# Optimization experiments

Measured on AMD Instinct MI355X. Metric: run time of the kernel, lower is better.

The kernel has to match this reference:

```python
import jax, jax.numpy as jnp
import numpy as np

HIDDEN = 2048
HEADS = 16
HEAD_DIM = HIDDEN // HEADS

def setup_inputs() -> dict:
    key = jax.random.key(0)
    ks = jax.random.split(key, 9)
    B, S = 1, 4096
    scale = 1.0 / np.sqrt(HIDDEN)
    x = jax.random.normal(ks[0], (B, S, HIDDEN), dtype=jnp.float32)
    Wq = jax.random.normal(ks[1], (HIDDEN, HIDDEN), dtype=jnp.float32) * scale
    Wk = jax.random.normal(ks[2], (HIDDEN, HIDDEN), dtype=jnp.float32) * scale
    Wv = jax.random.normal(ks[3], (HIDDEN, HIDDEN), dtype=jnp.float32) * scale
    Wo = jax.random.normal(ks[4], (HIDDEN, HIDDEN), dtype=jnp.float32) * scale
    bq = jax.random.normal(ks[5], (HIDDEN,), dtype=jnp.float32) * 0.01
    bk = jax.random.normal(ks[6], (HIDDEN,), dtype=jnp.float32) * 0.01
    bv = jax.random.normal(ks[7], (HIDDEN,), dtype=jnp.float32) * 0.01
    bo = jax.random.normal(ks[8], (HIDDEN,), dtype=jnp.float32) * 0.01
    return {"x": x, "Wq": Wq, "bq": bq, "Wk": Wk, "bk": bk, "Wv": Wv, "bv": bv, "Wo": Wo, "bo": bo}

def reference(x, Wq, bq, Wk, bk, Wv, bv, Wo, bo):
    B, S, D = x.shape
    H, Hd = HEADS, HEAD_DIM
    # projections (nn.Linear: x @ W^T + b)
    Q = (x @ Wq.T + bq).reshape(B, S, H, Hd).transpose(0, 2, 1, 3)  # [B,H,S,Hd]
    K = (x @ Wk.T + bk).reshape(B, S, H, Hd).transpose(0, 2, 1, 3)
    V = (x @ Wv.T + bv).reshape(B, S, H, Hd).transpose(0, 2, 1, 3)
    scores = jnp.einsum('bhqd,bhkd->bhqk', Q, K) / jnp.sqrt(jnp.float32(Hd))
    attn = jax.nn.softmax(scores, axis=-1)
    out = jnp.einsum('bhqk,bhkd->bhqd', attn, V)  # [B,H,S,Hd]
    out = out.transpose(0, 2, 1, 3).reshape(B, S, D)
    return out @ Wo.T + bo
```

## Files before the change

kernel.cpp:

```cpp
#include <hip/hip_runtime.h>

#define S_LEN  4096
#define DMODEL 2048
#define NHEADS 16
#define HDIM   128

typedef __bf16 bf16x8 __attribute__((ext_vector_type(8)));
typedef __bf16 bf16x2 __attribute__((ext_vector_type(2)));
typedef float  f32x4  __attribute__((ext_vector_type(4)));

__device__ __forceinline__ unsigned short f2b(float f) {
    unsigned int u = __float_as_uint(f);
    unsigned int r = (u + 0x7fffu + ((u >> 16) & 1u)) >> 16;
    return (unsigned short)r;
}

__device__ __forceinline__ unsigned int pkbf16(float a, float b) {
#if __has_builtin(__builtin_amdgcn_cvt_pk_bf16_f32)
    bf16x2 t = __builtin_amdgcn_cvt_pk_bf16_f32(a, b);
    return *(unsigned int*)&t;
#else
    return (unsigned int)f2b(a) | ((unsigned int)f2b(b) << 16);
#endif
}

__device__ __forceinline__ f32x4 mfma16(bf16x8 a, bf16x8 b, f32x4 c) {
    return __builtin_amdgcn_mfma_f32_16x16x32_bf16(a, b, c, 0, 0, 0);
}

__device__ __forceinline__ void ldg2lds16(const void* g, void* l) {
    __builtin_amdgcn_global_load_lds(
        (__attribute__((address_space(1))) void*)(void*)g,
        (__attribute__((address_space(3))) void*)l, 16, 0, 0);
}

__global__ __launch_bounds__(256) void cvt_bf16(
    const float* __restrict__ src, unsigned short* __restrict__ dst, int n4)
{
    int i = blockIdx.x * blockDim.x + threadIdx.x;
    if (i < n4) {
        float4 v = ((const float4*)src)[i];
        uint2 h;
        h.x = pkbf16(v.x, v.y); h.y = pkbf16(v.z, v.w);
        ((uint2*)dst)[i] = h;
    }
}

__global__ __launch_bounds__(256) void cvt_bf16_w4(
    const float* __restrict__ w0, const float* __restrict__ w1,
    const float* __restrict__ w2, const float* __restrict__ w3,
    unsigned short* __restrict__ d0, unsigned short* __restrict__ d1,
    unsigned short* __restrict__ d2, unsigned short* __restrict__ d3)
{
    const int z = blockIdx.y;
    const float* src = (z == 0) ? w0 : (z == 1) ? w1 : (z == 2) ? w2 : w3;
    unsigned short* dst = (z == 0) ? d0 : (z == 1) ? d1 : (z == 2) ? d2 : d3;
    int i = blockIdx.x * blockDim.x + threadIdx.x;
    float4 v = ((const float4*)src)[i];
    uint2 h;
    h.x = pkbf16(v.x, v.y); h.y = pkbf16(v.z, v.w);
    ((uint2*)dst)[i] = h;
}

__global__ __launch_bounds__(256, 2) void gemm_qkv(
    const unsigned short* __restrict__ xb,
    const unsigned short* __restrict__ Wqb, const float* __restrict__ bq,
    const unsigned short* __restrict__ Wkb, const float* __restrict__ bk,
    const unsigned short* __restrict__ Wvb, const float* __restrict__ bv,
    unsigned short* __restrict__ Qb, unsigned short* __restrict__ Kb,
    unsigned short* __restrict__ Vb)
{
    const int z = blockIdx.z;
    const unsigned short* B = (z == 0) ? Wqb : (z == 1) ? Wkb : Wvb;
    const float* bias        = (z == 0) ? bq  : (z == 1) ? bk  : bv;
    unsigned short* C        = (z == 0) ? Qb  : (z == 1) ? Kb  : Vb;
    const float oscale = (z == 0) ? 0.12751743f : 1.0f;

    __shared__ alignas(16) unsigned short As[128 * 32];
    __shared__ alignas(16) unsigned short Bs[128 * 32];

    const int tid = threadIdx.x;
    const int m0 = blockIdx.y * 128, n0 = blockIdx.x * 128;
    const int w = tid >> 6, lane = tid & 63, lo = lane & 15, qd = lane >> 4;
    const int wm = (w >> 1) * 64, wn = (w & 1) * 64;
    const int rsel = lane >> 2, csel = (lane & 3) * 8;

    f32x4 acc[4][4] = {};

    for (int k0 = 0; k0 < DMODEL; k0 += 32) {
#pragma unroll
        for (int i = 0; i < 2; i++) {
            int c = w * 2 + i;
            ldg2lds16(&xb[(size_t)(m0 + c * 16 + rsel) * DMODEL + k0 + csel],
                      &As[c * 512]);
            ldg2lds16(&B [(size_t)(n0 + c * 16 + rsel) * DMODEL + k0 + csel],
                      &Bs[c * 512]);
        }
        __syncthreads();

        bf16x8 af[4], bfr[4];
#pragma unroll
        for (int i = 0; i < 4; i++)
            af[i] = *(const bf16x8*)&As[(wm + i * 16 + lo) * 32 + qd * 8];
#pragma unroll
        for (int j = 0; j < 4; j++)
            bfr[j] = *(const bf16x8*)&Bs[(wn + j * 16 + lo) * 32 + qd * 8];
#pragma unroll
        for (int i = 0; i < 4; i++)
#pragma unroll
            for (int j = 0; j < 4; j++)
                acc[i][j] = mfma16(af[i], bfr[j], acc[i][j]);
        __syncthreads();
    }

#pragma unroll
    for (int j = 0; j < 4; j++) {
        int n = n0 + wn + j * 16 + lo;
        float bv_ = bias[n];
#pragma unroll
        for (int i = 0; i < 4; i++) {
#pragma unroll
            for (int r = 0; r < 4; r++) {
                int m = m0 + wm + i * 16 + qd * 4 + r;
                C[(size_t)m * DMODEL + n] = f2b((acc[i][j][r] + bv_) * oscale);
            }
        }
    }
}

__global__ __launch_bounds__(256, 2) void gemm_out(
    const unsigned short* __restrict__ Aatt, const unsigned short* __restrict__ Wob,
    const float* __restrict__ bo, float* __restrict__ out)
{
    __shared__ alignas(16) unsigned short As[128 * 32];
    __shared__ alignas(16) unsigned short Bs[128 * 32];

    const int tid = threadIdx.x;
    const int m0 = blockIdx.y * 128, n0 = blockIdx.x * 128;
    const int w = tid >> 6, lane = tid & 63, lo = lane & 15, qd = lane >> 4;
    const int wm = (w >> 1) * 64, wn = (w & 1) * 64;
    const int rsel = lane >> 2, csel = (lane & 3) * 8;

    f32x4 acc[4][4] = {};

    for (int k0 = 0; k0 < DMODEL; k0 += 32) {
#pragma unroll
        for (int i = 0; i < 2; i++) {
            int c = w * 2 + i;
            ldg2lds16(&Aatt[(size_t)(m0 + c * 16 + rsel) * DMODEL + k0 + csel],
                      &As[c * 512]);
            ldg2lds16(&Wob [(size_t)(n0 + c * 16 + rsel) * DMODEL + k0 + csel],
                      &Bs[c * 512]);
        }
        __syncthreads();

        bf16x8 af[4], bfr[4];
#pragma unroll
        for (int i = 0; i < 4; i++)
            af[i] = *(const bf16x8*)&As[(wm + i * 16 + lo) * 32 + qd * 8];
#pragma unroll
        for (int j = 0; j < 4; j++)
            bfr[j] = *(const bf16x8*)&Bs[(wn + j * 16 + lo) * 32 + qd * 8];
#pragma unroll
        for (int i = 0; i < 4; i++)
#pragma unroll
            for (int j = 0; j < 4; j++)
                acc[i][j] = mfma16(af[i], bfr[j], acc[i][j]);
        __syncthreads();
    }

#pragma unroll
    for (int j = 0; j < 4; j++) {
        int n = n0 + wn + j * 16 + lo;
        float bv_ = bo[n];
#pragma unroll
        for (int i = 0; i < 4; i++) {
#pragma unroll
            for (int r = 0; r < 4; r++) {
                int m = m0 + wm + i * 16 + qd * 4 + r;
                out[(size_t)m * DMODEL + n] = acc[i][j][r] + bv_;
            }
        }
    }
}

__global__ __launch_bounds__(256) void transpose_v(
    const unsigned short* __restrict__ Vb, unsigned short* __restrict__ Vt)
{
    __shared__ unsigned short tile[64 * 67];
    const int s0 = blockIdx.x * 64;
    const int d0 = blockIdx.y * 64;
    const int tid = threadIdx.x;
#pragma unroll
    for (int i = 0; i < 2; i++) {
        int chunk = tid + i * 256;
        int r = chunk >> 3, c8 = (chunk & 7) * 8;
        uint4 v = *(const uint4*)&Vb[(size_t)(s0 + r) * DMODEL + d0 + c8];
        const unsigned short* p = (const unsigned short*)&v;
#pragma unroll
        for (int j = 0; j < 8; j++) tile[r * 67 + c8 + j] = p[j];
    }
    __syncthreads();
#pragma unroll
    for (int i = 0; i < 2; i++) {
        int chunk = tid + i * 256;
        int r = chunk >> 3, c8 = (chunk & 7) * 8;
        unsigned short tmp[8];
#pragma unroll
        for (int j = 0; j < 8; j++) tmp[j] = tile[(c8 + j) * 67 + r];
        *(uint4*)&Vt[(size_t)(d0 + r) * S_LEN + s0 + c8] = *(uint4*)tmp;
    }
}

__global__ __launch_bounds__(256, 2) void attn_kernel(
    const unsigned short* __restrict__ Qb, const unsigned short* __restrict__ Kb,
    const unsigned short* __restrict__ Vt, unsigned short* __restrict__ Ob)
{
    const int id = blockIdx.x;
    const int xcd = id & 7, slot = id >> 3;
    const int h  = (xcd << 1) | (slot >> 5);
    const int q0 = (slot & 31) * 128;

    __shared__ alignas(16) unsigned short Ks[64 * 128];
    __shared__ alignas(16) unsigned short Vts[128 * 64];
    __shared__ alignas(16) unsigned short Ps[4][32 * 64];

    const int tid = threadIdx.x;
    const int w = tid >> 6, lane = tid & 63, lo = lane & 15, qd = lane >> 4;

    bf16x8 qf[2][4];
#pragma unroll
    for (int mt = 0; mt < 2; mt++) {
        const unsigned short* qrow =
            &Qb[(size_t)(q0 + w * 32 + mt * 16 + lo) * DMODEL + h * HDIM];
#pragma unroll
        for (int kk = 0; kk < 4; kk++)
            qf[mt][kk] = *(const bf16x8*)&qrow[kk * 32 + qd * 8];
    }

    f32x4 o_acc[2][8] = {};
    float l_run[2] = {0.f, 0.f};

    for (int kb = 0; kb < S_LEN / 64; kb++) {
        const int key0 = kb * 64;

#pragma unroll
        for (int i = 0; i < 4; i++) {
            int r = w * 16 + i * 4 + (lane >> 4);
            int c = (lane & 15) ^ (r & 7);
            ldg2lds16(&Kb[(size_t)(key0 + r) * DMODEL + h * HDIM + c * 8],
                      &Ks[(w * 16 + i * 4) * 128]);
        }
#pragma unroll
        for (int i = 0; i < 4; i++) {
            int r = w * 32 + i * 8 + (lane >> 3);
            int c = (lane & 7) ^ (r & 7);
            ldg2lds16(&Vt[(size_t)(h * HDIM + r) * S_LEN + key0 + c * 8],
                      &Vts[(w * 32 + i * 8) * 64]);
        }
        __syncthreads();

        f32x4 s[4][2] = {};
#pragma unroll
        for (int kk = 0; kk < 4; kk++) {
#pragma unroll
            for (int t = 0; t < 4; t++) {
                bf16x8 kf = *(const bf16x8*)
                    &Ks[(t * 16 + lo) * 128 + (((kk * 4 + qd) ^ (lo & 7)) * 8)];
                s[t][0] = mfma16(kf, qf[0][kk], s[t][0]);
                s[t][1] = mfma16(kf, qf[1][kk], s[t][1]);
            }
        }

#pragma unroll
        for (int mt = 0; mt < 2; mt++) {
            const int row = mt * 16 + lo;
            float lsum = 0.f;
#pragma unroll
            for (int t = 0; t < 4; t++) {
                float p0 = exp2f(s[t][mt][0]);
                float p1 = exp2f(s[t][mt][1]);
                float p2 = exp2f(s[t][mt][2]);
                float p3 = exp2f(s[t][mt][3]);
                lsum += (p0 + p1) + (p2 + p3);
                uint2 pkv;
                pkv.x = pkbf16(p0, p1);
                pkv.y = pkbf16(p2, p3);
                int swz = (t * 2 + (qd >> 1)) ^ (lo & 7);
                *(uint2*)&Ps[w][row * 64 + swz * 8 + (qd & 1) * 4] = pkv;
            }
            l_run[mt] += lsum;
        }
        asm volatile("s_waitcnt lgkmcnt(0)" ::: "memory");

#pragma unroll
        for (int kk = 0; kk < 2; kk++) {
            bf16x8 pf[2];
#pragma unroll
            for (int mt = 0; mt < 2; mt++)
                pf[mt] = *(const bf16x8*)
                    &Ps[w][(mt * 16 + lo) * 64 + (((kk * 4 + qd) ^ (lo & 7)) * 8)];
#pragma unroll
            for (int dt = 0; dt < 8; dt++) {
                bf16x8 vf = *(const bf16x8*)
                    &Vts[(dt * 16 + lo) * 64 + (((kk * 4 + qd) ^ (lo & 7)) * 8)];
                o_acc[0][dt] = mfma16(pf[0], vf, o_acc[0][dt]);
                o_acc[1][dt] = mfma16(pf[1], vf, o_acc[1][dt]);
            }
        }
        __syncthreads();
    }

#pragma unroll
    for (int mt = 0; mt < 2; mt++) {
        float l = l_run[mt];
        l += __shfl_xor(l, 16);
        l += __shfl_xor(l, 32);
        float inv_l[4];
#pragma unroll
        for (int r = 0; r < 4; r++)
            inv_l[r] = 1.0f / __shfl(l, qd * 4 + r);
#pragma unroll
        for (int dt = 0; dt < 8; dt++) {
#pragma unroll
            for (int r = 0; r < 4; r++) {
                int row = q0 + w * 32 + mt * 16 + qd * 4 + r;
                int col = h * HDIM + dt * 16 + lo;
                Ob[(size_t)row * DMODEL + col] = f2b(o_acc[mt][dt][r] * inv_l[r]);
            }
        }
    }
}

extern "C" void kernel_launch(void* const* d_in, const int* in_sizes, int n_in,
                              void* d_out, int out_size, void* d_ws, size_t ws_size,
                              hipStream_t stream)
{
    const float* x  = (const float*)d_in[0];
    const float* Wq = (const float*)d_in[1];
    const float* bq = (const float*)d_in[2];
    const float* Wk = (const float*)d_in[3];
    const float* bk = (const float*)d_in[4];
    const float* Wv = (const float*)d_in[5];
    const float* bv = (const float*)d_in[6];
    const float* Wo = (const float*)d_in[7];
    const float* bo = (const float*)d_in[8];
    float* out = (float*)d_out;

    const size_t N = (size_t)S_LEN * DMODEL;
    const size_t W = (size_t)DMODEL * DMODEL;
    unsigned short* Qb  = (unsigned short*)d_ws;
    unsigned short* Kb  = Qb + N;
    unsigned short* Vb  = Kb + N;
    unsigned short* xbv = Vb + N;
    unsigned short* Wqb = xbv + N;
    unsigned short* Wkb = Wqb + W;
    unsigned short* Wvb = Wkb + W;
    unsigned short* Wob = Wvb + W;
    unsigned short* Vt  = xbv;
    unsigned short* Ob  = Vb;

    cvt_bf16<<<(int)(N / 4 / 256), 256, 0, stream>>>(x, xbv, (int)(N / 4));
    cvt_bf16_w4<<<dim3((unsigned)(W / 4 / 256), 4), 256, 0, stream>>>(
        Wq, Wk, Wv, Wo, Wqb, Wkb, Wvb, Wob);

    gemm_qkv<<<dim3(DMODEL / 128, S_LEN / 128, 3), 256, 0, stream>>>(
        xbv, Wqb, bq, Wkb, bk, Wvb, bv, Qb, Kb, Vb);

    transpose_v<<<dim3(S_LEN / 64, DMODEL / 64), 256, 0, stream>>>(Vb, Vt);

    attn_kernel<<<512, 256, 0, stream>>>(Qb, Kb, Vt, Ob);

    gemm_out<<<dim3(DMODEL / 128, S_LEN / 128), 256, 0, stream>>>(Ob, Wob, bo, out);
}
```

Baseline: 512.0 us.

## Double-buffer K/V tiles in attention loop and raise wave priority around MFMAs

Splits the K and V shared-memory tiles into two buffers so the next block's global-to-LDS loads are issued before the current block's compute, overlapping memory latency with MFMA work. This drops one barrier per iteration. It also wraps the MFMA sections with s_setprio to favour the compute phase. LDS use roughly doubles for K/V, which may cut the two-blocks-per-CU occupancy. Correctness depends on the async LDS loads having completed before the barrier.

New measurement: 512.0 us. No clear change (-0.0%).

```diff
diff --git a/kernel.cpp b/kernel.cpp
--- a/kernel.cpp
+++ b/kernel.cpp
@@ -221,8 +221,8 @@
     const int h  = (xcd << 1) | (slot >> 5);
     const int q0 = (slot & 31) * 128;
 
-    __shared__ alignas(16) unsigned short Ks[64 * 128];
-    __shared__ alignas(16) unsigned short Vts[128 * 64];
+    __shared__ alignas(16) unsigned short Ks[2][64 * 128];
+    __shared__ alignas(16) unsigned short Vts[2][128 * 64];
     __shared__ alignas(16) unsigned short Ps[4][32 * 64];
 
     const int tid = threadIdx.x;
@@ -241,36 +241,48 @@
     f32x4 o_acc[2][8] = {};
     float l_run[2] = {0.f, 0.f};
 
+#define STAGE_KV(key0_, KsB_, VtsB_)                                          \
+    {                                                                         \
+        _Pragma("unroll")                                                     \
+        for (int i = 0; i < 4; i++) {                                         \
+            int r = w * 16 + i * 4 + (lane >> 4);                             \
+            int c = (lane & 15) ^ (r & 7);                                    \
+            ldg2lds16(&Kb[(size_t)((key0_) + r) * DMODEL + h * HDIM + c * 8], \
+                      &(KsB_)[(w * 16 + i * 4) * 128]);                       \
+        }                                                                     \
+        _Pragma("unroll")                                                     \
+        for (int i = 0; i < 4; i++) {                                         \
+            int r = w * 32 + i * 8 + (lane >> 3);                             \
+            int c = (lane & 7) ^ (r & 7);                                     \
+            ldg2lds16(&Vt[(size_t)(h * HDIM + r) * S_LEN + (key0_) + c * 8],  \
+                      &(VtsB_)[(w * 32 + i * 8) * 64]);                       \
+        }                                                                     \
+    }
+
+    STAGE_KV(0, Ks[0], Vts[0]);
+    __syncthreads();
+
+    int cur = 0;
     for (int kb = 0; kb < S_LEN / 64; kb++) {
-        const int key0 = kb * 64;
-
-#pragma unroll
-        for (int i = 0; i < 4; i++) {
-            int r = w * 16 + i * 4 + (lane >> 4);
-            int c = (lane & 15) ^ (r & 7);
-            ldg2lds16(&Kb[(size_t)(key0 + r) * DMODEL + h * HDIM + c * 8],
-                      &Ks[(w * 16 + i * 4) * 128]);
-        }
-#pragma unroll
-        for (int i = 0; i < 4; i++) {
-            int r = w * 32 + i * 8 + (lane >> 3);
-            int c = (lane & 7) ^ (r & 7);
-            ldg2lds16(&Vt[(size_t)(h * HDIM + r) * S_LEN + key0 + c * 8],
-                      &Vts[(w * 32 + i * 8) * 64]);
-        }
-        __syncthreads();
+        if (kb + 1 < S_LEN / 64)
+            STAGE_KV((kb + 1) * 64, Ks[cur ^ 1], Vts[cur ^ 1]);
+
+        const unsigned short* KsC  = Ks[cur];
+        const unsigned short* VtsC = Vts[cur];
 
         f32x4 s[4][2] = {};
+        __builtin_amdgcn_s_setprio(1);
 #pragma unroll
         for (int kk = 0; kk < 4; kk++) {
 #pragma unroll
             for (int t = 0; t < 4; t++) {
                 bf16x8 kf = *(const bf16x8*)
-                    &Ks[(t * 16 + lo) * 128 + (((kk * 4 + qd) ^ (lo & 7)) * 8)];
+                    &KsC[(t * 16 + lo) * 128 + (((kk * 4 + qd) ^ (lo & 7)) * 8)];
                 s[t][0] = mfma16(kf, qf[0][kk], s[t][0]);
                 s[t][1] = mfma16(kf, qf[1][kk], s[t][1]);
             }
         }
+        __builtin_amdgcn_s_setprio(0);
 
 #pragma unroll
         for (int mt = 0; mt < 2; mt++) {
@@ -293,6 +305,7 @@
         }
         asm volatile("s_waitcnt lgkmcnt(0)" ::: "memory");
 
+        __builtin_amdgcn_s_setprio(1);
 #pragma unroll
         for (int kk = 0; kk < 2; kk++) {
             bf16x8 pf[2];
@@ -303,13 +316,17 @@
 #pragma unroll
             for (int dt = 0; dt < 8; dt++) {
                 bf16x8 vf = *(const bf16x8*)
-                    &Vts[(dt * 16 + lo) * 64 + (((kk * 4 + qd) ^ (lo & 7)) * 8)];
+                    &VtsC[(dt * 16 + lo) * 64 + (((kk * 4 + qd) ^ (lo & 7)) * 8)];
                 o_acc[0][dt] = mfma16(pf[0], vf, o_acc[0][dt]);
                 o_acc[1][dt] = mfma16(pf[1], vf, o_acc[1][dt]);
             }
         }
-        __syncthreads();
-    }
+        __builtin_amdgcn_s_setprio(0);
+
+        __syncthreads();
+        cur ^= 1;
+    }
+#undef STAGE_KV
 
 #pragma unroll
     for (int mt = 0; mt < 2; mt++) {
```

## Halve attention query tile to 64 rows and double grid for occupancy

Applied to the files above, without the earlier changes.

Each attention block now handles 64 query rows (16 per wave) instead of 128, so 1024 blocks launch and launch bounds allow 4 blocks per CU. This cuts accumulator registers per wave to raise occupancy and spread work across more CUs. The cost is that each K/V tile loaded into LDS is reused by half as many queries, doubling global K/V traffic. The change also raises wave priority around the MFMA sections and switches to the raw hardware exp2 builtin.

After: 507.2 us. Within noise of the previous version (-0.9%).

```diff
diff --git a/kernel.cpp b/kernel.cpp
--- a/kernel.cpp
+++ b/kernel.cpp
@@ -212,34 +212,33 @@
     }
 }
 
-__global__ __launch_bounds__(256, 2) void attn_kernel(
+__global__ __launch_bounds__(256, 4) void attn_kernel(
     const unsigned short* __restrict__ Qb, const unsigned short* __restrict__ Kb,
     const unsigned short* __restrict__ Vt, unsigned short* __restrict__ Ob)
 {
     const int id = blockIdx.x;
     const int xcd = id & 7, slot = id >> 3;
-    const int h  = (xcd << 1) | (slot >> 5);
-    const int q0 = (slot & 31) * 128;
+    const int h  = (xcd << 1) | (slot >> 6);
+    const int q0 = (slot & 63) * 64;
 
     __shared__ alignas(16) unsigned short Ks[64 * 128];
     __shared__ alignas(16) unsigned short Vts[128 * 64];
-    __shared__ alignas(16) unsigned short Ps[4][32 * 64];
+    __shared__ alignas(16) unsigned short Ps[4][16 * 64];
 
     const int tid = threadIdx.x;
     const int w = tid >> 6, lane = tid & 63, lo = lane & 15, qd = lane >> 4;
 
-    bf16x8 qf[2][4];
-#pragma unroll
-    for (int mt = 0; mt < 2; mt++) {
+    bf16x8 qf[4];
+    {
         const unsigned short* qrow =
-            &Qb[(size_t)(q0 + w * 32 + mt * 16 + lo) * DMODEL + h * HDIM];
+            &Qb[(size_t)(q0 + w * 16 + lo) * DMODEL + h * HDIM];
 #pragma unroll
         for (int kk = 0; kk < 4; kk++)
-            qf[mt][kk] = *(const bf16x8*)&qrow[kk * 32 + qd * 8];
-    }
-
-    f32x4 o_acc[2][8] = {};
-    float l_run[2] = {0.f, 0.f};
+            qf[kk] = *(const bf16x8*)&qrow[kk * 32 + qd * 8];
+    }
+
+    f32x4 o_acc[8] = {};
+    float l_run = 0.f;
 
     for (int kb = 0; kb < S_LEN / 64; kb++) {
         const int key0 = kb * 64;
@@ -260,28 +259,28 @@
         }
         __syncthreads();
 
-        f32x4 s[4][2] = {};
+        f32x4 s[4] = {};
+        __builtin_amdgcn_s_setprio(1);
 #pragma unroll
         for (int kk = 0; kk < 4; kk++) {
 #pragma unroll
             for (int t = 0; t < 4; t++) {
                 bf16x8 kf = *(const bf16x8*)
                     &Ks[(t * 16 + lo) * 128 + (((kk * 4 + qd) ^ (lo & 7)) * 8)];
-                s[t][0] = mfma16(kf, qf[0][kk], s[t][0]);
-                s[t][1] = mfma16(kf, qf[1][kk], s[t][1]);
-            }
-        }
-
-#pragma unroll
-        for (int mt = 0; mt < 2; mt++) {
-            const int row = mt * 16 + lo;
+                s[t] = mfma16(kf, qf[kk], s[t]);
+            }
+        }
+        __builtin_amdgcn_s_setprio(0);
+
+        {
+            const int row = lo;
             float lsum = 0.f;
 #pragma unroll
             for (int t = 0; t < 4; t++) {
-                float p0 = exp2f(s[t][mt][0]);
-                float p1 = exp2f(s[t][mt][1]);
-                float p2 = exp2f(s[t][mt][2]);
-                float p3 = exp2f(s[t][mt][3]);
+                float p0 = __builtin_amdgcn_exp2f(s[t][0]);
+                float p1 = __builtin_amdgcn_exp2f(s[t][1]);
+                float p2 = __builtin_amdgcn_exp2f(s[t][2]);
+                float p3 = __builtin_amdgcn_exp2f(s[t][3]);
                 lsum += (p0 + p1) + (p2 + p3);
                 uint2 pkv;
                 pkv.x = pkbf16(p0, p1);
@@ -289,31 +288,29 @@
                 int swz = (t * 2 + (qd >> 1)) ^ (lo & 7);
                 *(uint2*)&Ps[w][row * 64 + swz * 8 + (qd & 1) * 4] = pkv;
             }
-            l_run[mt] += lsum;
+            l_run += lsum;
         }
         asm volatile("s_waitcnt lgkmcnt(0)" ::: "memory");
 
+        __builtin_amdgcn_s_setprio(1);
 #pragma unroll
         for (int kk = 0; kk < 2; kk++) {
-            bf16x8 pf[2];
-#pragma unroll
-            for (int mt = 0; mt < 2; mt++)
-                pf[mt] = *(const bf16x8*)
-                    &Ps[w][(mt * 16 + lo) * 64 + (((kk * 4 + qd) ^ (lo & 7)) * 8)];
+            bf16x8 pf = *(const bf16x8*)
+                &Ps[w][lo * 64 + (((kk * 4 + qd) ^ (lo & 7)) * 8)];
 #pragma unroll
             for (int dt = 0; dt < 8; dt++) {
                 bf16x8 vf = *(const bf16x8*)
                     &Vts[(dt * 16 + lo) * 64 + (((kk * 4 + qd) ^ (lo & 7)) * 8)];
-                o_acc[0][dt] = mfma16(pf[0], vf, o_acc[0][dt]);
-                o_acc[1][dt] = mfma16(pf[1], vf, o_acc[1][dt]);
-            }
-        }
-        __syncthreads();
-    }
-
-#pragma unroll
-    for (int mt = 0; mt < 2; mt++) {
-        float l = l_run[mt];
+                o_acc[dt] = mfma16(pf, vf, o_acc[dt]);
+            }
+        }
+        __builtin_amdgcn_s_setprio(0);
+
+        __syncthreads();
+    }
+
+    {
+        float l = l_run;
         l += __shfl_xor(l, 16);
         l += __shfl_xor(l, 32);
         float inv_l[4];
@@ -324,9 +321,9 @@
         for (int dt = 0; dt < 8; dt++) {
 #pragma unroll
             for (int r = 0; r < 4; r++) {
-                int row = q0 + w * 32 + mt * 16 + qd * 4 + r;
+                int row = q0 + w * 16 + qd * 4 + r;
                 int col = h * HDIM + dt * 16 + lo;
-                Ob[(size_t)row * DMODEL + col] = f2b(o_acc[mt][dt][r] * inv_l[r]);
+                Ob[(size_t)row * DMODEL + col] = f2b(o_acc[dt][r] * inv_l[r]);
             }
         }
     }
@@ -369,7 +366,7 @@
 
     transpose_v<<<dim3(S_LEN / 64, DMODEL / 64), 256, 0, stream>>>(Vb, Vt);
 
-    attn_kernel<<<512, 256, 0, stream>>>(Qb, Kb, Vt, Ob);
+    attn_kernel<<<1024, 256, 0, stream>>>(Qb, Kb, Vt, Ob);
 
     gemm_out<<<dim3(DMODEL / 128, S_LEN / 128), 256, 0, stream>>>(Ob, Wob, bo, out);
 }
```
